# Kernel tuning notes

Measured on AMD Instinct MI355X. Metric: run time of the kernel, lower is better.

Reference implementation:

```python
import jax, jax.numpy as jnp
import numpy as np

B, T, D, H, O = 1024, 16, 1024, 2048, 1024
BETA, TAU, THR, EPS = 0.9, 2.0, 1.0, 1e-5


def setup_inputs() -> dict:
    key = jax.random.key(0)
    ks = jax.random.split(key, 12)
    def lin(kw, kb, fan_in, fan_out):
        bound = 1.0 / np.sqrt(fan_in)
        W = jax.random.uniform(kw, (fan_in, fan_out), minval=-bound, maxval=bound, dtype=jnp.float32)
        b = jax.random.uniform(kb, (fan_out,), minval=-bound, maxval=bound, dtype=jnp.float32)
        return W, b
    x = jax.random.uniform(ks[0], (B, T, D), dtype=jnp.float32)  # spike-rate-like input, skips encoder
    Wp, bp = lin(ks[1], ks[2], D, H)        # input_proj
    Wfc, bfc = lin(ks[3], ks[4], H, H)      # recursive_layer.fc
    gamma = jnp.ones((H,), jnp.float32)     # recursive_layer.norm
    beta_ln = jnp.zeros((H,), jnp.float32)
    Wg, bg = lin(ks[5], ks[6], H, H)        # controller.gate
    Wenc, benc = lin(ks[7], ks[8], H, H)    # LSA.encoding_weights
    Wrec, brec = lin(ks[9], ks[10], H, H)   # LSA.recurrent_weights
    Wro, bro = lin(ks[11], jax.random.fold_in(key, 99), H, O)  # readout
    return dict(x=x, Wp=Wp, bp=bp, Wfc=Wfc, bfc=bfc, gamma=gamma, beta_ln=beta_ln,
                Wg=Wg, bg=bg, Wenc=Wenc, benc=benc, Wrec=Wrec, brec=brec, Wro=Wro, bro=bro)


def reference(x, Wp, bp, Wfc, bfc, gamma, beta_ln, Wg, bg, Wenc, benc, Wrec, brec, Wro, bro):
    dt = x.dtype
    b = x.shape[0]
    h = Wp.shape[1]

    def ln(v):
        m = v.mean(-1, keepdims=True)
        var = v.var(-1, keepdims=True)  # biased, matches torch LayerNorm
        return (v - m) / jnp.sqrt(var + EPS) * gamma + beta_ln

    # hoist the input projection out of the recurrence: [B,T,D]@[D,H] -> [T,B,H]
    inp_all = jnp.swapaxes(jnp.einsum('btd,dh->bth', x, Wp) + bp, 0, 1)

    def step(carry, inp):
        rec, attr = carry
        # RecursiveMeaningLayer
        update = jnp.tanh(inp @ Wfc + bfc)
        new_rec = BETA * rec + (1.0 - BETA) * update
        ctx = ln(new_rec)
        # RecursionController
        g = jax.nn.sigmoid((ctx + new_rec) @ Wg + bg)
        gated = g * ctx + (1.0 - g) * new_rec
        # LegendreSpikeAttractor
        current = gated @ Wenc + benc + attr @ Wrec + brec
        new_v = attr + (current - attr) / TAU
        spikes = (new_v > THR).astype(dt)
        new_attr = new_v - spikes * THR
        return (new_rec, new_attr), spikes

    init = (jnp.zeros((b, h), dt), jnp.zeros((b, h), dt))
    (rec, attr), spk = jax.lax.scan(step, init, inp_all)  # spk: [T,B,H]
    features = spk.mean(axis=0)
    out = features @ Wro + bro
    return out, rec, attr
```

## Files before the change

kernel.cpp:

```cpp
#include <hip/hip_runtime.h>
#include <math.h>


#define BB 1024
#define TT 16
#define DD 1024
#define HH 2048
#define OO 1024

typedef double d4 __attribute__((ext_vector_type(4)));

struct RdF {
    const float* p; long ld;
    __device__ double operator()(int r, int c) const { return (double)p[(long)r*ld + c]; }
};
struct RdD {
    const double* p; long ld;
    __device__ double operator()(int r, int c) const { return p[(long)r*ld + c]; }
};
struct RdSum {
    const double* a; const double* b; long ld;
    __device__ double operator()(int r, int c) const { long i=(long)r*ld+c; return a[i]+b[i]; }
};
struct RdSpk {
    const float* p; long ld;
    __device__ double operator()(int r, int c) const { return (double)p[(long)r*ld+c] * 0.0625; }
};

#define LDAS 65
#define LDBS 65
#define TILE_A (32*LDAS)
#define TILE_B (32*LDBS)
#define LDS_DBL (2*(TILE_A + TILE_B))

template<typename AR, typename BR>
__device__ __forceinline__ void gemm_mfma(AR A, BR B, int row0, int col0, int K,
                                          double* __restrict__ S,
                                          d4 acc[2][2])
{
    const int tid  = threadIdx.x;
    const int lane = tid & 63;
    const int wid  = tid >> 6;
    const int wm   = wid >> 1;
    const int wn   = wid & 1;
    const int l15  = lane & 15;
    const int l4   = lane >> 4;
    const int am = tid >> 2, ak = (tid & 3) << 3;
    const int bk = tid >> 3, bn = (tid & 7) << 3;

    double* A0 = S;
    double* B0 = S + TILE_A;
    double* A1 = S + TILE_A + TILE_B;
    double* B1 = A1 + TILE_A;

    double ar[8], br[8];
    #pragma unroll
    for (int j = 0; j < 8; ++j) ar[j] = A(row0 + am, ak + j);
    #pragma unroll
    for (int j = 0; j < 8; ++j) br[j] = B(bk, col0 + bn + j);

    __syncthreads();
    #pragma unroll
    for (int j = 0; j < 8; ++j) A0[(ak + j)*LDAS + am] = ar[j];
    #pragma unroll
    for (int j = 0; j < 8; ++j) B0[bk*LDBS + bn + j] = br[j];
    __syncthreads();

    double *cA = A0, *cB = B0, *nA = A1, *nB = B1;
    const int nt = K >> 5;
    for (int t = 0; t < nt; ++t) {
        if (t + 1 < nt) {
            #pragma unroll
            for (int j = 0; j < 8; ++j) ar[j] = A(row0 + am, (t+1)*32 + ak + j);
            #pragma unroll
            for (int j = 0; j < 8; ++j) br[j] = B((t+1)*32 + bk, col0 + bn + j);
        }
        #pragma unroll
        for (int ks = 0; ks < 8; ++ks) {
            const int kk = ks*4 + l4;
            double a0 = cA[kk*LDAS + wm*32 +      l15];
            double a1 = cA[kk*LDAS + wm*32 + 16 + l15];
            double b0 = cB[kk*LDBS + wn*32 +      l15];
            double b1 = cB[kk*LDBS + wn*32 + 16 + l15];
            acc[0][0] = __builtin_amdgcn_mfma_f64_16x16x4f64(a0, b0, acc[0][0], 0, 0, 0);
            acc[0][1] = __builtin_amdgcn_mfma_f64_16x16x4f64(a0, b1, acc[0][1], 0, 0, 0);
            acc[1][0] = __builtin_amdgcn_mfma_f64_16x16x4f64(a1, b0, acc[1][0], 0, 0, 0);
            acc[1][1] = __builtin_amdgcn_mfma_f64_16x16x4f64(a1, b1, acc[1][1], 0, 0, 0);
        }
        if (t + 1 < nt) {
            #pragma unroll
            for (int j = 0; j < 8; ++j) nA[(ak + j)*LDAS + am] = ar[j];
            #pragma unroll
            for (int j = 0; j < 8; ++j) nB[bk*LDBS + bn + j] = br[j];
            __syncthreads();
            double* x;
            x = cA; cA = nA; nA = x;
            x = cB; cB = nB; nB = x;
        }
    }
}

#define GEMM_EPILOG_VARS                                   \
    const int lane = threadIdx.x & 63;                     \
    const int wid  = threadIdx.x >> 6;                     \
    const int wm   = wid >> 1, wn = wid & 1;               \
    const int l15  = lane & 15, l4 = lane >> 4;

__global__ __launch_bounds__(256) void k_wpf(const float* __restrict__ Wp,
                                             const float* __restrict__ Wfc,
                                             double* __restrict__ Wpf)
{
    __shared__ double S[LDS_DBL];
    d4 acc[2][2] = {};
    int row0 = blockIdx.y*64, col0 = blockIdx.x*64;
    gemm_mfma(RdF{Wp, HH}, RdF{Wfc, HH}, row0, col0, HH, S, acc);
    GEMM_EPILOG_VARS
    #pragma unroll
    for (int i=0;i<2;i++)
      #pragma unroll
      for (int j=0;j<2;j++)
        #pragma unroll
        for (int r=0;r<4;r++) {
            int d = row0 + wm*32 + i*16 + l4 + 4*r;
            int h = col0 + wn*32 + j*16 + l15;
            Wpf[(long)d*HH + h] = acc[i][j][r];
        }
}

__global__ __launch_bounds__(256) void k_bpf(const float* __restrict__ bp,
                                             const float* __restrict__ Wfc,
                                             const float* __restrict__ bfc,
                                             double* __restrict__ bpf)
{
    int h = blockIdx.x*256 + threadIdx.x;
    double acc = 0.0;
    for (int k = 0; k < HH; ++k)
        acc = fma((double)bp[k], (double)Wfc[(long)k*HH + h], acc);
    bpf[h] = acc + (double)bfc[h];
}

__global__ __launch_bounds__(256) void k_update(const float* __restrict__ x, int t,
                                                const double* __restrict__ Wpf,
                                                const double* __restrict__ bpf,
                                                double* __restrict__ rec)
{
    __shared__ double S[LDS_DBL];
    d4 acc[2][2] = {};
    int row0 = blockIdx.y*64, col0 = blockIdx.x*64;
    const float* x_t = x + (long)t*DD;
    gemm_mfma(RdF{x_t, (long)TT*DD}, RdD{Wpf, HH}, row0, col0, DD, S, acc);
    GEMM_EPILOG_VARS
    const double BETA = 0.9;
    const double OMB  = 1.0 - BETA;
    #pragma unroll
    for (int i=0;i<2;i++)
      #pragma unroll
      for (int j=0;j<2;j++)
        #pragma unroll
        for (int r=0;r<4;r++) {
            int b = row0 + wm*32 + i*16 + l4 + 4*r;
            int h = col0 + wn*32 + j*16 + l15;
            double u = tanh(acc[i][j][r] + bpf[h]);
            long idx = (long)b*HH + h;
            rec[idx] = BETA*rec[idx] + OMB*u;
        }
}

__global__ __launch_bounds__(256) void k_ln(const double* __restrict__ rec,
                                            const float* __restrict__ gamma,
                                            const float* __restrict__ beta,
                                            double* __restrict__ ctx)
{
    __shared__ double red[256];
    int b = blockIdx.x, tid = threadIdx.x;
    const double* r = rec + (long)b*HH;
    double s = 0.0;
    for (int h = tid; h < HH; h += 256) s += r[h];
    red[tid] = s; __syncthreads();
    for (int off = 128; off > 0; off >>= 1) {
        if (tid < off) red[tid] += red[tid+off];
        __syncthreads();
    }
    double mean = red[0] / HH;
    __syncthreads();
    double v = 0.0;
    for (int h = tid; h < HH; h += 256) { double d = r[h]-mean; v += d*d; }
    red[tid] = v; __syncthreads();
    for (int off = 128; off > 0; off >>= 1) {
        if (tid < off) red[tid] += red[tid+off];
        __syncthreads();
    }
    double sd = sqrt(red[0] / HH + 1e-5);
    for (int h = tid; h < HH; h += 256) {
        long idx = (long)b*HH + h;
        ctx[idx] = (r[h]-mean)/sd * (double)gamma[h] + (double)beta[h];
    }
}

__global__ __launch_bounds__(256) void k_gate(const double* __restrict__ ctx,
                                              const double* __restrict__ rec,
                                              const float* __restrict__ Wg,
                                              const float* __restrict__ bg,
                                              double* __restrict__ gated)
{
    __shared__ double S[LDS_DBL];
    d4 acc[2][2] = {};
    int row0 = blockIdx.y*64, col0 = blockIdx.x*64;
    gemm_mfma(RdSum{ctx, rec, HH}, RdF{Wg, HH}, row0, col0, HH, S, acc);
    GEMM_EPILOG_VARS
    #pragma unroll
    for (int i=0;i<2;i++)
      #pragma unroll
      for (int j=0;j<2;j++)
        #pragma unroll
        for (int r=0;r<4;r++) {
            int b = row0 + wm*32 + i*16 + l4 + 4*r;
            int h = col0 + wn*32 + j*16 + l15;
            long idx = (long)b*HH + h;
            double g = 1.0/(1.0 + exp(-(acc[i][j][r] + (double)bg[h])));
            gated[idx] = g*ctx[idx] + (1.0-g)*rec[idx];
        }
}

__global__ __launch_bounds__(256) void k_current(const double* __restrict__ gated,
                                                 const float* __restrict__ Wenc,
                                                 const double* __restrict__ attr_in,
                                                 const float* __restrict__ Wrec,
                                                 const float* __restrict__ benc,
                                                 const float* __restrict__ brec,
                                                 double* __restrict__ attr_out,
                                                 float* __restrict__ spkcnt)
{
    __shared__ double S[LDS_DBL];
    d4 acc[2][2] = {};
    int row0 = blockIdx.y*64, col0 = blockIdx.x*64;
    gemm_mfma(RdD{gated,   HH}, RdF{Wenc, HH}, row0, col0, HH, S, acc);
    gemm_mfma(RdD{attr_in, HH}, RdF{Wrec, HH}, row0, col0, HH, S, acc);
    GEMM_EPILOG_VARS
    const double TAU = 2.0, THR = 1.0;
    #pragma unroll
    for (int i=0;i<2;i++)
      #pragma unroll
      for (int j=0;j<2;j++)
        #pragma unroll
        for (int r=0;r<4;r++) {
            int b = row0 + wm*32 + i*16 + l4 + 4*r;
            int h = col0 + wn*32 + j*16 + l15;
            long idx = (long)b*HH + h;
            double cur = acc[i][j][r] + (double)benc[h] + (double)brec[h];
            double a   = attr_in[idx];
            double nv  = a + (cur - a)/TAU;
            double sp  = (nv > THR) ? 1.0 : 0.0;
            attr_out[idx] = nv - sp*THR;
            spkcnt[idx] += (float)sp;
        }
}

__global__ __launch_bounds__(256) void k_readout(const float* __restrict__ spkcnt,
                                                 const float* __restrict__ Wro,
                                                 const float* __restrict__ bro,
                                                 float* __restrict__ out)
{
    __shared__ double S[LDS_DBL];
    d4 acc[2][2] = {};
    int row0 = blockIdx.y*64, col0 = blockIdx.x*64;
    gemm_mfma(RdSpk{spkcnt, HH}, RdF{Wro, OO}, row0, col0, HH, S, acc);
    GEMM_EPILOG_VARS
    #pragma unroll
    for (int i=0;i<2;i++)
      #pragma unroll
      for (int j=0;j<2;j++)
        #pragma unroll
        for (int r=0;r<4;r++) {
            int b = row0 + wm*32 + i*16 + l4 + 4*r;
            int o = col0 + wn*32 + j*16 + l15;
            out[(long)b*OO + o] = (float)(acc[i][j][r] + (double)bro[o]);
        }
}

__global__ __launch_bounds__(256) void k_d2f(const double* __restrict__ src,
                                             float* __restrict__ dst)
{
    long i = (long)blockIdx.x*256 + threadIdx.x;
    dst[i] = (float)src[i];
}

extern "C" void kernel_launch(void* const* d_in, const int* in_sizes, int n_in,
                              void* d_out, int out_size, void* d_ws, size_t ws_size,
                              hipStream_t stream) {
    const float* x    = (const float*)d_in[0];
    const float* Wp   = (const float*)d_in[1];
    const float* bp   = (const float*)d_in[2];
    const float* Wfc  = (const float*)d_in[3];
    const float* bfc  = (const float*)d_in[4];
    const float* gamma= (const float*)d_in[5];
    const float* beta = (const float*)d_in[6];
    const float* Wg   = (const float*)d_in[7];
    const float* bg   = (const float*)d_in[8];
    const float* Wenc = (const float*)d_in[9];
    const float* benc = (const float*)d_in[10];
    const float* Wrec = (const float*)d_in[11];
    const float* brec = (const float*)d_in[12];
    const float* Wro  = (const float*)d_in[13];
    const float* bro  = (const float*)d_in[14];
    float* out = (float*)d_out;

    const long NBH = (long)BB*HH;
    char* p = (char*)d_ws;
    double* Wpf   = (double*)p; p += (long)DD*HH*sizeof(double);
    double* bpf   = (double*)p; p += HH*sizeof(double);
    double* rec   = (double*)p; p += NBH*sizeof(double);
    double* attrA = (double*)p; p += NBH*sizeof(double);
    double* attrB = (double*)p; p += NBH*sizeof(double);
    double* ctx   = (double*)p; p += NBH*sizeof(double);
    double* gated = (double*)p; p += NBH*sizeof(double);
    float*  spkcnt= (float*)p;  p += NBH*sizeof(float);

    hipMemsetAsync(rec,    0, NBH*sizeof(double), stream);
    hipMemsetAsync(attrA,  0, NBH*sizeof(double), stream);
    hipMemsetAsync(spkcnt, 0, NBH*sizeof(float),  stream);

    dim3 blk(256);
    dim3 g_wpf(HH/64, DD/64);
    k_wpf<<<g_wpf, blk, 0, stream>>>(Wp, Wfc, Wpf);
    k_bpf<<<HH/256, blk, 0, stream>>>(bp, Wfc, bfc, bpf);

    dim3 g_step(HH/64, BB/64);
    double* ain  = attrA;
    double* aout = attrB;
    for (int t = 0; t < TT; ++t) {
        k_update <<<g_step, blk, 0, stream>>>(x, t, Wpf, bpf, rec);
        k_ln     <<<BB,     blk, 0, stream>>>(rec, gamma, beta, ctx);
        k_gate   <<<g_step, blk, 0, stream>>>(ctx, rec, Wg, bg, gated);
        k_current<<<g_step, blk, 0, stream>>>(gated, Wenc, ain, Wrec, benc, brec, aout, spkcnt);
        double* tmp = ain; ain = aout; aout = tmp;
    }

    dim3 g_ro(OO/64, BB/64);
    k_readout<<<g_ro, blk, 0, stream>>>(spkcnt, Wro, bro, out);
    k_d2f<<<NBH/256, blk, 0, stream>>>(rec, out + (long)BB*OO);
    k_d2f<<<NBH/256, blk, 0, stream>>>(ain, out + (long)BB*OO + NBH);
}
```

Baseline: 10.33 ms.

## Split gate/current GEMMs across K, stage fp32 B tiles, swizzle blocks

The gate and current GEMMs are split along K (gate) or across the two matmuls (current) into a z=2 grid that writes partial sums. Separate elementwise kernels then combine the partials and apply the sigmoid or LIF epilogue. This doubles the number of blocks per launch to fill the GPU better. B operands stay as fp32 in LDS, halving shared memory so three blocks can fit per CU, and block indices are swizzled for L2 locality. In exchange there are extra global round-trips for the partials and two more launches per timestep, and scratch buffers (aout, ctx) are reused for the partials.

Measured after the change: 10.02 ms. 1.03x faster.

```diff
diff --git a/kernel.cpp b/kernel.cpp
--- a/kernel.cpp
+++ b/kernel.cpp
@@ -29,14 +29,94 @@
 
 #define LDAS 65
 #define LDBS 65
-#define TILE_A (32*LDAS)
-#define TILE_B (32*LDBS)
-#define LDS_DBL (2*(TILE_A + TILE_B))
+#define LDBF 72
+
+template<typename AR>
+__device__ __forceinline__ void gemm32(AR A, const float* __restrict__ Bp, long ldb,
+                                       int row0, int col0, int kbase, int K,
+                                       double* __restrict__ Asd,
+                                       float*  __restrict__ Bsf,
+                                       d4 acc[2][2])
+{
+    const int tid  = threadIdx.x;
+    const int lane = tid & 63;
+    const int wid  = tid >> 6;
+    const int wm   = wid >> 1;
+    const int wn   = wid & 1;
+    const int l15  = lane & 15;
+    const int l4   = lane >> 4;
+    const int am = tid >> 2, ak = (tid & 3) << 3;
+    const int bkb = wid << 3;
+    const int brr = lane >> 5;
+    const int bc  = (lane & 31) << 1;
+
+    double* A0 = Asd;           double* A1 = Asd + 32*LDAS;
+    float*  B0 = Bsf;           float*  B1 = Bsf + 32*LDBF;
+
+    double ar[8]; float2 br[4];
+    #pragma unroll
+    for (int j = 0; j < 8; ++j) ar[j] = A(row0 + am, kbase + ak + j);
+    #pragma unroll
+    for (int j = 0; j < 4; ++j) {
+        int rw = bkb + 2*j + brr;
+        br[j] = *(const float2*)(Bp + (long)(kbase + rw)*ldb + col0 + bc);
+    }
+    __syncthreads();
+    #pragma unroll
+    for (int j = 0; j < 8; ++j) A0[(ak + j)*LDAS + am] = ar[j];
+    #pragma unroll
+    for (int j = 0; j < 4; ++j) {
+        int rw = bkb + 2*j + brr;
+        *(float2*)(B0 + rw*LDBF + bc) = br[j];
+    }
+    __syncthreads();
+
+    double *cA = A0, *nA = A1;
+    float  *cB = B0, *nB = B1;
+    const int nt = K >> 5;
+    for (int t = 0; t < nt; ++t) {
+        if (t + 1 < nt) {
+            #pragma unroll
+            for (int j = 0; j < 8; ++j) ar[j] = A(row0 + am, kbase + (t+1)*32 + ak + j);
+            #pragma unroll
+            for (int j = 0; j < 4; ++j) {
+                int rw = bkb + 2*j + brr;
+                br[j] = *(const float2*)(Bp + (long)(kbase + (t+1)*32 + rw)*ldb + col0 + bc);
+            }
+        }
+        #pragma unroll
+        for (int ks = 0; ks < 8; ++ks) {
+            const int kk = ks*4 + l4;
+            double a0 = cA[kk*LDAS + wm*32 +      l15];
+            double a1 = cA[kk*LDAS + wm*32 + 16 + l15];
+            double b0 = (double)cB[kk*LDBF + wn*32 +      l15];
+            double b1 = (double)cB[kk*LDBF + wn*32 + 16 + l15];
+            acc[0][0] = __builtin_amdgcn_mfma_f64_16x16x4f64(a0, b0, acc[0][0], 0, 0, 0);
+            acc[0][1] = __builtin_amdgcn_mfma_f64_16x16x4f64(a0, b1, acc[0][1], 0, 0, 0);
+            acc[1][0] = __builtin_amdgcn_mfma_f64_16x16x4f64(a1, b0, acc[1][0], 0, 0, 0);
+            acc[1][1] = __builtin_amdgcn_mfma_f64_16x16x4f64(a1, b1, acc[1][1], 0, 0, 0);
+        }
+        if (t + 1 < nt) {
+            #pragma unroll
+            for (int j = 0; j < 8; ++j) nA[(ak + j)*LDAS + am] = ar[j];
+            #pragma unroll
+            for (int j = 0; j < 4; ++j) {
+                int rw = bkb + 2*j + brr;
+                *(float2*)(nB + rw*LDBF + bc) = br[j];
+            }
+            __syncthreads();
+            double* xd; float* xf;
+            xd = cA; cA = nA; nA = xd;
+            xf = cB; cB = nB; nB = xf;
+        }
+    }
+}
 
 template<typename AR, typename BR>
-__device__ __forceinline__ void gemm_mfma(AR A, BR B, int row0, int col0, int K,
-                                          double* __restrict__ S,
-                                          d4 acc[2][2])
+__device__ __forceinline__ void gemm64(AR A, BR B, int row0, int col0, int K,
+                                       double* __restrict__ Asd,
+                                       double* __restrict__ Bsd,
+                                       d4 acc[2][2])
 {
     const int tid  = threadIdx.x;
     const int lane = tid & 63;
@@ -48,10 +128,8 @@
     const int am = tid >> 2, ak = (tid & 3) << 3;
     const int bk = tid >> 3, bn = (tid & 7) << 3;
 
-    double* A0 = S;
-    double* B0 = S + TILE_A;
-    double* A1 = S + TILE_A + TILE_B;
-    double* B1 = A1 + TILE_A;
+    double* A0 = Asd; double* A1 = Asd + 32*LDAS;
+    double* B0 = Bsd; double* B1 = Bsd + 32*LDBS;
 
     double ar[8], br[8];
     #pragma unroll
@@ -106,14 +184,24 @@
     const int wm   = wid >> 1, wn = wid & 1;               \
     const int l15  = lane & 15, l4 = lane >> 4;
 
-__global__ __launch_bounds__(256) void k_wpf(const float* __restrict__ Wp,
-                                             const float* __restrict__ Wfc,
-                                             double* __restrict__ Wpf)
-{
-    __shared__ double S[LDS_DBL];
+__device__ __forceinline__ void swz3216(int& bx, int& by) {
+    int id = bx + (by << 5);
+    int k = id & 7, t = id >> 3;
+    bx = ((k & 3) << 3) + (t & 7);
+    by = ((k >> 2) << 3) + (t >> 3);
+}
+
+__global__ __launch_bounds__(256, 3) void k_wpf(const float* __restrict__ Wp,
+                                                const float* __restrict__ Wfc,
+                                                double* __restrict__ Wpf)
+{
+    __shared__ double Asd[2*32*LDAS];
+    __shared__ float  Bsf[2*32*LDBF];
     d4 acc[2][2] = {};
-    int row0 = blockIdx.y*64, col0 = blockIdx.x*64;
-    gemm_mfma(RdF{Wp, HH}, RdF{Wfc, HH}, row0, col0, HH, S, acc);
+    int bx = blockIdx.x, by = blockIdx.y;
+    swz3216(bx, by);
+    int row0 = by*64, col0 = bx*64;
+    gemm32(RdF{Wp, HH}, Wfc, HH, row0, col0, 0, HH, Asd, Bsf, acc);
     GEMM_EPILOG_VARS
     #pragma unroll
     for (int i=0;i<2;i++)
@@ -144,11 +232,14 @@
                                                 const double* __restrict__ bpf,
                                                 double* __restrict__ rec)
 {
-    __shared__ double S[LDS_DBL];
+    __shared__ double Asd[2*32*LDAS];
+    __shared__ double Bsd[2*32*LDBS];
     d4 acc[2][2] = {};
-    int row0 = blockIdx.y*64, col0 = blockIdx.x*64;
+    int bx = blockIdx.x, by = blockIdx.y;
+    swz3216(bx, by);
+    int row0 = by*64, col0 = bx*64;
     const float* x_t = x + (long)t*DD;
-    gemm_mfma(RdF{x_t, (long)TT*DD}, RdD{Wpf, HH}, row0, col0, DD, S, acc);
+    gemm64(RdF{x_t, (long)TT*DD}, RdD{Wpf, HH}, row0, col0, DD, Asd, Bsd, acc);
     GEMM_EPILOG_VARS
     const double BETA = 0.9;
     const double OMB  = 1.0 - BETA;
@@ -197,16 +288,20 @@
     }
 }
 
-__global__ __launch_bounds__(256) void k_gate(const double* __restrict__ ctx,
-                                              const double* __restrict__ rec,
-                                              const float* __restrict__ Wg,
-                                              const float* __restrict__ bg,
-                                              double* __restrict__ gated)
-{
-    __shared__ double S[LDS_DBL];
+__global__ __launch_bounds__(256, 3) void k_gate_part(const double* __restrict__ ctx,
+                                                      const double* __restrict__ rec,
+                                                      const float* __restrict__ Wg,
+                                                      double* __restrict__ p0,
+                                                      double* __restrict__ p1)
+{
+    __shared__ double Asd[2*32*LDAS];
+    __shared__ float  Bsf[2*32*LDBF];
     d4 acc[2][2] = {};
-    int row0 = blockIdx.y*64, col0 = blockIdx.x*64;
-    gemm_mfma(RdSum{ctx, rec, HH}, RdF{Wg, HH}, row0, col0, HH, S, acc);
+    int bx = blockIdx.x, by = blockIdx.y, z = blockIdx.z;
+    swz3216(bx, by);
+    int row0 = by*64, col0 = bx*64;
+    gemm32(RdSum{ctx, rec, HH}, Wg, HH, row0, col0, z*1024, 1024, Asd, Bsf, acc);
+    double* P = z ? p1 : p0;
     GEMM_EPILOG_VARS
     #pragma unroll
     for (int i=0;i<2;i++)
@@ -216,28 +311,41 @@
         for (int r=0;r<4;r++) {
             int b = row0 + wm*32 + i*16 + l4 + 4*r;
             int h = col0 + wn*32 + j*16 + l15;
-            long idx = (long)b*HH + h;
-            double g = 1.0/(1.0 + exp(-(acc[i][j][r] + (double)bg[h])));
-            gated[idx] = g*ctx[idx] + (1.0-g)*rec[idx];
-        }
-}
-
-__global__ __launch_bounds__(256) void k_current(const double* __restrict__ gated,
-                                                 const float* __restrict__ Wenc,
-                                                 const double* __restrict__ attr_in,
-                                                 const float* __restrict__ Wrec,
-                                                 const float* __restrict__ benc,
-                                                 const float* __restrict__ brec,
-                                                 double* __restrict__ attr_out,
-                                                 float* __restrict__ spkcnt)
-{
-    __shared__ double S[LDS_DBL];
+            P[(long)b*HH + h] = acc[i][j][r];
+        }
+}
+
+__global__ __launch_bounds__(256) void k_gatefin(const double* __restrict__ p0,
+                                                 const double* __restrict__ ctx,
+                                                 const double* __restrict__ rec,
+                                                 const float* __restrict__ bg,
+                                                 double* __restrict__ gated)
+{
+    long i = (long)blockIdx.x*256 + threadIdx.x;
+    int h = (int)(i & (HH-1));
+    double s = p0[i] + gated[i] + (double)bg[h];
+    double g = 1.0/(1.0 + exp(-s));
+    gated[i] = g*ctx[i] + (1.0-g)*rec[i];
+}
+
+__global__ __launch_bounds__(256, 3) void k_current_part(const double* __restrict__ gated,
+                                                         const float* __restrict__ Wenc,
+                                                         const double* __restrict__ attr_in,
+                                                         const float* __restrict__ Wrec,
+                                                         double* __restrict__ p0,
+                                                         double* __restrict__ p1)
+{
+    __shared__ double Asd[2*32*LDAS];
+    __shared__ float  Bsf[2*32*LDBF];
     d4 acc[2][2] = {};
-    int row0 = blockIdx.y*64, col0 = blockIdx.x*64;
-    gemm_mfma(RdD{gated,   HH}, RdF{Wenc, HH}, row0, col0, HH, S, acc);
-    gemm_mfma(RdD{attr_in, HH}, RdF{Wrec, HH}, row0, col0, HH, S, acc);
+    int bx = blockIdx.x, by = blockIdx.y, z = blockIdx.z;
+    swz3216(bx, by);
+    int row0 = by*64, col0 = bx*64;
+    const double* Ap = z ? attr_in : gated;
+    const float*  Bp = z ? Wrec    : Wenc;
+    double*       Cp = z ? p1      : p0;
+    gemm32(RdD{Ap, HH}, Bp, HH, row0, col0, 0, HH, Asd, Bsf, acc);
     GEMM_EPILOG_VARS
-    const double TAU = 2.0, THR = 1.0;
     #pragma unroll
     for (int i=0;i<2;i++)
       #pragma unroll
@@ -246,25 +354,38 @@
         for (int r=0;r<4;r++) {
             int b = row0 + wm*32 + i*16 + l4 + 4*r;
             int h = col0 + wn*32 + j*16 + l15;
-            long idx = (long)b*HH + h;
-            double cur = acc[i][j][r] + (double)benc[h] + (double)brec[h];
-            double a   = attr_in[idx];
-            double nv  = a + (cur - a)/TAU;
-            double sp  = (nv > THR) ? 1.0 : 0.0;
-            attr_out[idx] = nv - sp*THR;
-            spkcnt[idx] += (float)sp;
-        }
-}
-
-__global__ __launch_bounds__(256) void k_readout(const float* __restrict__ spkcnt,
-                                                 const float* __restrict__ Wro,
-                                                 const float* __restrict__ bro,
-                                                 float* __restrict__ out)
-{
-    __shared__ double S[LDS_DBL];
+            Cp[(long)b*HH + h] = acc[i][j][r];
+        }
+}
+
+__global__ __launch_bounds__(256) void k_lif(const double* __restrict__ p0,
+                                             const double* __restrict__ attr_in,
+                                             const float* __restrict__ benc,
+                                             const float* __restrict__ brec,
+                                             double* __restrict__ attr_out,
+                                             float* __restrict__ spkcnt)
+{
+    long i = (long)blockIdx.x*256 + threadIdx.x;
+    int h = (int)(i & (HH-1));
+    const double TAU = 2.0, THR = 1.0;
+    double cur = p0[i] + attr_out[i] + (double)benc[h] + (double)brec[h];
+    double a   = attr_in[i];
+    double nv  = a + (cur - a)/TAU;
+    double sp  = (nv > THR) ? 1.0 : 0.0;
+    attr_out[i] = nv - sp*THR;
+    spkcnt[i] += (float)sp;
+}
+
+__global__ __launch_bounds__(256, 3) void k_readout(const float* __restrict__ spkcnt,
+                                                    const float* __restrict__ Wro,
+                                                    const float* __restrict__ bro,
+                                                    float* __restrict__ out)
+{
+    __shared__ double Asd[2*32*LDAS];
+    __shared__ float  Bsf[2*32*LDBF];
     d4 acc[2][2] = {};
     int row0 = blockIdx.y*64, col0 = blockIdx.x*64;
-    gemm_mfma(RdSpk{spkcnt, HH}, RdF{Wro, OO}, row0, col0, HH, S, acc);
+    gemm32(RdSpk{spkcnt, HH}, Wro, OO, row0, col0, 0, HH, Asd, Bsf, acc);
     GEMM_EPILOG_VARS
     #pragma unroll
     for (int i=0;i<2;i++)
@@ -325,14 +446,18 @@
     k_wpf<<<g_wpf, blk, 0, stream>>>(Wp, Wfc, Wpf);
     k_bpf<<<HH/256, blk, 0, stream>>>(bp, Wfc, bfc, bpf);
 
-    dim3 g_step(HH/64, BB/64);
+    dim3 g_step (HH/64, BB/64);
+    dim3 g_split(HH/64, BB/64, 2);
+    const int NEW = (int)(NBH/256);
     double* ain  = attrA;
     double* aout = attrB;
     for (int t = 0; t < TT; ++t) {
         k_update <<<g_step, blk, 0, stream>>>(x, t, Wpf, bpf, rec);
         k_ln     <<<BB,     blk, 0, stream>>>(rec, gamma, beta, ctx);
-        k_gate   <<<g_step, blk, 0, stream>>>(ctx, rec, Wg, bg, gated);
-        k_current<<<g_step, blk, 0, stream>>>(gated, Wenc, ain, Wrec, benc, brec, aout, spkcnt);
+        k_gate_part<<<g_split, blk, 0, stream>>>(ctx, rec, Wg, aout, gated);
+        k_gatefin  <<<NEW,     blk, 0, stream>>>(aout, ctx, rec, bg, gated);
+        k_current_part<<<g_split, blk, 0, stream>>>(gated, Wenc, ain, Wrec, ctx, aout);
+        k_lif         <<<NEW,     blk, 0, stream>>>(ctx, ain, benc, brec, aout, spkcnt);
         double* tmp = ain; ain = aout; aout = tmp;
     }
 
```
